# Kernel optimization log

Measured on AMD Instinct MI355X. Metric: run time of the kernel, lower is better.

## Reference

```python
import jax, jax.numpy as jnp
import numpy as np

EPS = 1e-6


def setup_inputs() -> dict:
    key = jax.random.key(0)
    ks = jax.random.split(key, 6)
    B, T, C, H, D, M = 1, 2048, 1024, 16, 64, 64
    return {
        "x": jax.random.normal(ks[0], (B, T, C), dtype=jnp.float32),
        "w_qkv": jax.random.normal(ks[1], (C, 3 * C), dtype=jnp.float32) * (1.0 / np.sqrt(C)),
        "b_qkv": jax.random.normal(ks[2], (3 * C,), dtype=jnp.float32) * 0.02,
        "w_out": jax.random.normal(ks[3], (C, C), dtype=jnp.float32) * (1.0 / np.sqrt(C)),
        "b_out": jax.random.normal(ks[4], (C,), dtype=jnp.float32) * 0.02,
        "proj": jax.random.normal(ks[5], (H, D, M), dtype=jnp.float32),
    }


def _feature_map(x, proj):
    # x: [B,H,T,D], proj: [H,D,M] -> [B,H,T,M]
    M = proj.shape[-1]
    p = jnp.einsum("bhtd,hdm->bhtm", x, proj)
    return jax.nn.relu(p) / jnp.sqrt(jnp.float32(M))


def reference(x, w_qkv, b_qkv, w_out, b_out, proj):
    B, T, C = x.shape
    H, D, M = proj.shape
    qkv = x @ w_qkv + b_qkv                        # [B,T,3C]
    q, k, v = jnp.split(qkv, 3, axis=-1)
    # [B,T,C] -> [B,H,T,D]
    to_heads = lambda t: t.reshape(B, T, H, D).transpose(0, 2, 1, 3)
    q, k, v = to_heads(q), to_heads(k), to_heads(v)

    q_prime = _feature_map(q, proj)                # [B,H,T,M]
    k_prime = _feature_map(k, proj)                # [B,H,T,M]

    # causal linear attention: cumulative sum of outer products k' v^T
    kv_prod = jnp.einsum("bhtm,bhtd->bhtmd", k_prime, v)   # [B,H,T,M,D]
    kv_cumsum = jnp.cumsum(kv_prod, axis=2)
    context = jnp.einsum("bhtm,bhtmd->bhtd", q_prime, kv_cumsum)

    k_cumsum = jnp.cumsum(k_prime, axis=2)                   # [B,H,T,M]
    norm = jnp.einsum("bhtm,bhtm->bht", q_prime, k_cumsum)
    out = context / (norm[..., None] + EPS)                  # [B,H,T,D]

    out = out.transpose(0, 2, 1, 3).reshape(B, T, C)
    return out @ w_out + b_out
```

## Files before the change

### kernel.cpp

```cpp
#include <hip/hip_runtime.h>
#include <hip/hip_bf16.h>

#define TT 2048
#define CC 1024
#define HH 16
#define DD 64
#define FM 64
#define NCH 32
#define CL 64
#define N_QKV 3072
#define EPSV 1e-6f

#define OFF_KS  0u
#define OFF_Z   32768u
#define OFF_U16 65536u
#define U_KVT 0u
#define U_PROJT 2097152u
#define U_VT  6291456u
#define U_QP  8388608u
#define U_KP  10485760u
#define U_ST  12582912u
#define U_XBF 14680064u
#define U_WQT 16777216u
#define U_WOT 19922944u

typedef __attribute__((ext_vector_type(8))) short bf16x8;
typedef __attribute__((ext_vector_type(4))) float f32x4;
typedef __attribute__((ext_vector_type(4))) unsigned short u16x4;

__device__ __forceinline__ unsigned short f2bf(float f) {
  unsigned int u = __float_as_uint(f);
  u = (u + 0x7fffu + ((u >> 16) & 1u)) >> 16;
  return (unsigned short)u;
}
__device__ __forceinline__ float bf2f(unsigned short b) {
  return __uint_as_float(((unsigned)b) << 16);
}

__device__ __forceinline__ void gload16(const void* g, void* l) {
  __builtin_amdgcn_global_load_lds(
      (const __attribute__((address_space(1))) unsigned int*)g,
      (__attribute__((address_space(3))) unsigned int*)l, 16, 0, 0);
}

__device__ __forceinline__ void stage_tile64(const unsigned short* g, unsigned rowstride,
                                             unsigned short* lds, int w, int lane) {
  const int l8 = lane >> 3, l7 = lane & 7;
  const int kcg = (l7 ^ l8) * 8;
#pragma unroll
  for (int jj = 0; jj < 2; ++jj) {
    const int inst = w * 2 + jj;
    const int row = inst * 8 + l8;
    gload16(&g[(unsigned)row * rowstride + kcg], &lds[inst * 512]);
  }
}

__device__ __forceinline__ bf16x8 frag64(const unsigned short* lds, int r, int kchunk) {
  const int slot = kchunk ^ (r & 7);
  return *reinterpret_cast<const bf16x8*>(&lds[r * 64 + slot * 8]);
}

__device__ __forceinline__ void transpose64_dev(const float* __restrict__ src,
                                                unsigned short* __restrict__ dst,
                                                int K, int N, int k0, int n0,
                                                float (*T)[68], int tid) {
#pragma unroll
  for (int it = 0; it < 4; ++it) {
    int f = tid + it * 256;
    int r = f >> 4, c4 = (f & 15) * 4;
    float4 v = *reinterpret_cast<const float4*>(&src[(unsigned)(k0 + r) * N + n0 + c4]);
    T[r][c4 + 0] = v.x; T[r][c4 + 1] = v.y;
    T[r][c4 + 2] = v.z; T[r][c4 + 3] = v.w;
  }
  __syncthreads();
#pragma unroll
  for (int it = 0; it < 4; ++it) {
    int f = tid + it * 256;
    int nl = f >> 4, kq = (f & 15) * 4;
    u16x4 o;
#pragma unroll
    for (int j = 0; j < 4; ++j) o[j] = f2bf(T[kq + j][nl]);
    *reinterpret_cast<u16x4*>(&dst[(unsigned)(n0 + nl) * K + k0 + kq]) = o;
  }
}

__global__ __launch_bounds__(256) void k_prep(const float* __restrict__ x,
                                              const float* __restrict__ wq,
                                              const float* __restrict__ wo,
                                              const float* __restrict__ proj,
                                              unsigned short* __restrict__ xbf,
                                              unsigned short* __restrict__ wqT,
                                              unsigned short* __restrict__ woT,
                                              unsigned short* __restrict__ projT) {
  __shared__ float T[64][68];
  const int tid = threadIdx.x;
  int b = blockIdx.x;
  if (b < 2048) {
    unsigned i = (unsigned)b * 1024u + (unsigned)tid * 4u;
    float4 v = *reinterpret_cast<const float4*>(&x[i]);
    u16x4 o;
    o[0] = f2bf(v.x); o[1] = f2bf(v.y); o[2] = f2bf(v.z); o[3] = f2bf(v.w);
    *reinterpret_cast<u16x4*>(&xbf[i]) = o;
    return;
  }
  b -= 2048;
  if (b < 768) {
    transpose64_dev(wq, wqT, CC, N_QKV, (b / 48) * 64, (b % 48) * 64, T, tid);
    return;
  }
  b -= 768;
  if (b < 256) {
    transpose64_dev(wo, woT, CC, CC, (b / 16) * 64, (b % 16) * 64, T, tid);
    return;
  }
  b -= 256;
  transpose64_dev(proj + (unsigned)b * 4096u, projT + (unsigned)b * 4096u, 64, 64, 0, 0, T, tid);
}

__global__ __launch_bounds__(256) void k_qkv_mfma(const unsigned short* __restrict__ Xbf,
                                                  const unsigned short* __restrict__ WqT,
                                                  const float* __restrict__ bias,
                                                  const unsigned short* __restrict__ projT,
                                                  unsigned short* __restrict__ qp,
                                                  unsigned short* __restrict__ kp,
                                                  unsigned short* __restrict__ vt) {
  __shared__ unsigned short LDSU[12288];
  unsigned short* As = LDSU;
  unsigned short* Bs = LDSU + 4096;
  const int tid = threadIdx.x, lane = tid & 63, w = tid >> 6;
  const int wm = w >> 1, wn = w & 1;
  int lin = blockIdx.y * 24 + blockIdx.x;
  int swz = (lin & 7) * 96 + (lin >> 3);
  const int bx = swz % 24, by = swz / 24;
  const int m0b = by * 64, n0b = bx * 128;
  const int l8 = lane >> 3, l7 = lane & 7;
  const int kcg = (l7 ^ l8) * 8;
  f32x4 acc[2][4] = {};
  for (int k0 = 0; k0 < CC; k0 += 64) {
    if (k0) __syncthreads();
#pragma unroll
    for (int jj = 0; jj < 2; ++jj) {
      const int inst = w * 2 + jj;
      const int row = inst * 8 + l8;
      gload16(&Xbf[(unsigned)(m0b + row) * CC + k0 + kcg], &As[inst * 512]);
    }
#pragma unroll
    for (int jj = 0; jj < 4; ++jj) {
      const int inst = w * 4 + jj;
      const int row = inst * 8 + l8;
      gload16(&WqT[(unsigned)(n0b + row) * CC + k0 + kcg], &Bs[inst * 512]);
    }
    __syncthreads();
#pragma unroll
    for (int kk = 0; kk < 2; ++kk) {
      bf16x8 af[2], bg[4];
#pragma unroll
      for (int i = 0; i < 2; ++i) {
        const int r = wm * 32 + i * 16 + (lane & 15);
        const int slot = (kk * 4 + (lane >> 4)) ^ (r & 7);
        af[i] = *reinterpret_cast<const bf16x8*>(&As[r * 64 + slot * 8]);
      }
#pragma unroll
      for (int j = 0; j < 4; ++j) {
        const int r = wn * 64 + j * 16 + (lane & 15);
        const int slot = (kk * 4 + (lane >> 4)) ^ (r & 7);
        bg[j] = *reinterpret_cast<const bf16x8*>(&Bs[r * 64 + slot * 8]);
      }
#pragma unroll
      for (int i = 0; i < 2; ++i)
#pragma unroll
        for (int j = 0; j < 4; ++j)
          acc[i][j] = __builtin_amdgcn_mfma_f32_16x16x32_bf16(af[i], bg[j],
                                                              acc[i][j], 0, 0, 0);
    }
  }
  const int n0w = n0b + wn * 64;
  const int sel = n0w >> 10;
  const int h = (n0w & 1023) >> 6;
  const int t0w = m0b + wm * 32;
  float bvj[4];
#pragma unroll
  for (int j = 0; j < 4; ++j) bvj[j] = bias[n0w + j * 16 + (lane & 15)];
  __syncthreads();
  unsigned short* myT = LDSU + w * 2048;
#pragma unroll
  for (int i = 0; i < 2; ++i)
#pragma unroll
    for (int j = 0; j < 4; ++j) {
      const int d = j * 16 + (lane & 15);
#pragma unroll
      for (int r = 0; r < 4; ++r) {
        const int t = i * 16 + (lane >> 4) * 4 + r;
        myT[t * 64 + (((d >> 3) ^ (t & 7)) << 3) + (d & 7)] = f2bf(acc[i][j][r] + bvj[j]);
      }
    }
  if (sel == 2) {
#pragma unroll
    for (int q = 0; q < 4; ++q) {
      const int cid = q * 64 + lane;
      const int d = cid >> 2, tc = cid & 3;
      bf16x8 o;
#pragma unroll
      for (int e = 0; e < 8; ++e) {
        const int t = tc * 8 + e;
        o[e] = (short)myT[t * 64 + (((d >> 3) ^ (t & 7)) << 3) + (d & 7)];
      }
      *reinterpret_cast<bf16x8*>(&vt[((unsigned)h * 64 + d) * TT + t0w + tc * 8]) = o;
    }
    return;
  }
  const unsigned short* pjt = projT + (unsigned)h * 4096u;
  bf16x8 aq[2][2], bp[4][2];
#pragma unroll
  for (int jm = 0; jm < 4; ++jm)
#pragma unroll
    for (int kk = 0; kk < 2; ++kk)
      bp[jm][kk] = *reinterpret_cast<const bf16x8*>(
          &pjt[(unsigned)(jm * 16 + (lane & 15)) * 64 + kk * 32 + (lane >> 4) * 8]);
#pragma unroll
  for (int i = 0; i < 2; ++i)
#pragma unroll
    for (int kk = 0; kk < 2; ++kk)
      aq[i][kk] = frag64(myT, i * 16 + (lane & 15), kk * 4 + (lane >> 4));
  f32x4 accp[2][4] = {};
#pragma unroll
  for (int i = 0; i < 2; ++i)
#pragma unroll
    for (int jm = 0; jm < 4; ++jm)
#pragma unroll
      for (int kk = 0; kk < 2; ++kk)
        accp[i][jm] = __builtin_amdgcn_mfma_f32_16x16x32_bf16(aq[i][kk], bp[jm][kk],
                                                              accp[i][jm], 0, 0, 0);
#pragma unroll
  for (int i = 0; i < 2; ++i)
#pragma unroll
    for (int jm = 0; jm < 4; ++jm) {
      const int m = jm * 16 + (lane & 15);
#pragma unroll
      for (int r = 0; r < 4; ++r) {
        const int t = i * 16 + (lane >> 4) * 4 + r;
        float v = accp[i][jm][r];
        v = (v > 0.f ? v : 0.f) * 0.125f;
        myT[t * 64 + (((m >> 3) ^ (t & 7)) << 3) + (m & 7)] = f2bf(v);
      }
    }
  unsigned short* dst0 = (sel ? kp : qp) + ((unsigned)h * TT + (unsigned)t0w) * 64u;
#pragma unroll
  for (int q = 0; q < 4; ++q) {
    const int cid = q * 64 + lane;
    const int t = cid >> 3, mc = cid & 7;
    bf16x8 o = *reinterpret_cast<const bf16x8*>(&myT[t * 64 + ((mc ^ (t & 7)) << 3)]);
    *reinterpret_cast<bf16x8*>(&dst0[(unsigned)cid * 8]) = o;
  }
}

__global__ __launch_bounds__(256) void k_chunkkv(const unsigned short* __restrict__ kp,
                                                 const unsigned short* __restrict__ vt,
                                                 unsigned short* __restrict__ kvt,
                                                 float* __restrict__ ksum) {
  __shared__ unsigned short Xs[4096];
  __shared__ unsigned short VTs[4096];
  const int tid = threadIdx.x, lane = tid & 63, w = tid >> 6;
  const int c = blockIdx.x, h = blockIdx.y;
  stage_tile64(kp + ((unsigned)h * TT + c * 64) * 64, 64, Xs, w, lane);
  stage_tile64(vt + (unsigned)h * 64 * TT + (unsigned)c * 64, TT, VTs, w, lane);
  __syncthreads();
  const int m = w * 16 + (lane & 15);
  bf16x8 afm[2];
  float ks = 0.f;
#pragma unroll
  for (int kk = 0; kk < 2; ++kk)
#pragma unroll
    for (int e = 0; e < 8; ++e) {
      const int t = kk * 32 + (lane >> 4) * 8 + e;
      unsigned short u = Xs[t * 64 + (((m >> 3) ^ (t & 7)) << 3) + (m & 7)];
      afm[kk][e] = (short)u;
      ks += bf2f(u);
    }
  ks += __shfl_xor(ks, 16, 64);
  ks += __shfl_xor(ks, 32, 64);
  if (lane < 16) ksum[((unsigned)h * NCH + c) * 64u + m] = ks;
  f32x4 acckv[4] = {};
#pragma unroll
  for (int j = 0; j < 4; ++j)
#pragma unroll
    for (int kk = 0; kk < 2; ++kk)
      acckv[j] = __builtin_amdgcn_mfma_f32_16x16x32_bf16(
          afm[kk], frag64(VTs, j * 16 + (lane & 15), kk * 4 + (lane >> 4)), acckv[j], 0, 0, 0);
  unsigned short* dkv = kvt + ((unsigned)h * NCH + c) * 4096u;
#pragma unroll
  for (int j = 0; j < 4; ++j) {
    const int d = j * 16 + (lane & 15);
    const int mq = w * 16 + (lane >> 4) * 4;
    u16x4 o;
#pragma unroll
    for (int r = 0; r < 4; ++r) o[r] = f2bf(acckv[j][r]);
    *reinterpret_cast<u16x4*>(&dkv[(unsigned)d * 64 + mq]) = o;
  }
}

__global__ __launch_bounds__(256) void k_prefix(const unsigned short* __restrict__ kvt,
                                                const float* __restrict__ ksum,
                                                unsigned short* __restrict__ st,
                                                float* __restrict__ z) {
  const int h = blockIdx.y;
  const unsigned e = blockIdx.x * 256u + threadIdx.x;
  float run = 0.f;
#pragma unroll
  for (int c = 0; c < NCH; ++c) {
    const unsigned idx = ((unsigned)h * NCH + c) * 4096u + e;
    st[idx] = f2bf(run);
    run += bf2f(kvt[idx]);
  }
  if (blockIdx.x == 0 && threadIdx.x < 64) {
    float zr = 0.f;
#pragma unroll
    for (int c = 0; c < NCH; ++c) {
      const unsigned idx = ((unsigned)h * NCH + c) * 64u + threadIdx.x;
      z[idx] = zr;
      zr += ksum[idx];
    }
  }
}

__global__ __launch_bounds__(256) void k_attn(const unsigned short* __restrict__ qp,
                                              const unsigned short* __restrict__ kp,
                                              const unsigned short* __restrict__ vt,
                                              const unsigned short* __restrict__ st,
                                              const float* __restrict__ z,
                                              unsigned short* __restrict__ attnb) {
  __shared__ unsigned short QPs[4096];
  __shared__ unsigned short KPs[4096];
  __shared__ unsigned short VTs[4096];
  __shared__ unsigned short STs[4096];
  __shared__ float zsm[64];
  __shared__ float nsm[64];
  const int tid = threadIdx.x, lane = tid & 63, w = tid >> 6;
  const int c = blockIdx.x, h = blockIdx.y;
  stage_tile64(qp + ((unsigned)h * TT + c * 64) * 64, 64, QPs, w, lane);
  stage_tile64(kp + ((unsigned)h * TT + c * 64) * 64, 64, KPs, w, lane);
  stage_tile64(vt + (unsigned)h * 64 * TT + (unsigned)c * 64, TT, VTs, w, lane);
  stage_tile64(st + ((unsigned)h * NCH + c) * 4096u, 64, STs, w, lane);
  if (tid < 64) zsm[tid] = z[((unsigned)h * NCH + c) * 64u + tid];
  __syncthreads();
  const int tr = w * 16 + (lane & 15);
  bf16x8 afq[2];
#pragma unroll
  for (int kk = 0; kk < 2; ++kk) afq[kk] = frag64(QPs, tr, kk * 4 + (lane >> 4));
  f32x4 accA[4] = {};
#pragma unroll
  for (int j = 0; j < 4; ++j)
#pragma unroll
    for (int kk = 0; kk < 2; ++kk)
      accA[j] = __builtin_amdgcn_mfma_f32_16x16x32_bf16(
          afq[kk], frag64(KPs, j * 16 + (lane & 15), kk * 4 + (lane >> 4)), accA[j], 0, 0, 0);
  float rs[4] = {0.f, 0.f, 0.f, 0.f};
#pragma unroll
  for (int j = 0; j < 4; ++j) {
    const int s = j * 16 + (lane & 15);
#pragma unroll
    for (int r = 0; r < 4; ++r) {
      const int t = w * 16 + (lane >> 4) * 4 + r;
      float v = (s <= t) ? accA[j][r] : 0.f;
      accA[j][r] = v;
      rs[r] += v;
    }
  }
#pragma unroll
  for (int r = 0; r < 4; ++r)
#pragma unroll
    for (int off = 1; off < 16; off <<= 1) rs[r] += __shfl_xor(rs[r], off, 64);
  __syncthreads();
  if ((lane & 15) == 0) {
#pragma unroll
    for (int r = 0; r < 4; ++r) nsm[w * 16 + (lane >> 4) * 4 + r] = rs[r];
  }
#pragma unroll
  for (int j = 0; j < 4; ++j) {
    const int s = j * 16 + (lane & 15);
#pragma unroll
    for (int r = 0; r < 4; ++r) {
      const int t = w * 16 + (lane >> 4) * 4 + r;
      KPs[t * 64 + (((s >> 3) ^ (t & 7)) * 8) + (s & 7)] = f2bf(accA[j][r]);
    }
  }
  __syncthreads();
  {
    const int t = tid >> 2, part = tid & 3;
    float qz = 0.f;
#pragma unroll
    for (int mm = 0; mm < 16; ++mm) {
      const int m = part * 16 + mm;
      qz += bf2f(QPs[t * 64 + (((m >> 3) ^ (t & 7)) * 8) + (m & 7)]) * zsm[m];
    }
    qz += __shfl_xor(qz, 1, 64);
    qz += __shfl_xor(qz, 2, 64);
    if (part == 0) nsm[t] += qz + EPSV;
  }
  bf16x8 afa[2];
#pragma unroll
  for (int kk = 0; kk < 2; ++kk) afa[kk] = frag64(KPs, tr, kk * 4 + (lane >> 4));
  f32x4 acc[4] = {};
#pragma unroll
  for (int j = 0; j < 4; ++j) {
    const int br = j * 16 + (lane & 15);
#pragma unroll
    for (int kk = 0; kk < 2; ++kk) {
      acc[j] = __builtin_amdgcn_mfma_f32_16x16x32_bf16(
          afa[kk], frag64(VTs, br, kk * 4 + (lane >> 4)), acc[j], 0, 0, 0);
      acc[j] = __builtin_amdgcn_mfma_f32_16x16x32_bf16(
          afq[kk], frag64(STs, br, kk * 4 + (lane >> 4)), acc[j], 0, 0, 0);
    }
  }
  __syncthreads();
#pragma unroll
  for (int j = 0; j < 4; ++j) {
    const int d = j * 16 + (lane & 15);
#pragma unroll
    for (int r = 0; r < 4; ++r) {
      const int t = w * 16 + (lane >> 4) * 4 + r;
      attnb[(unsigned)(c * 64 + t) * CC + h * 64 + d] = f2bf(acc[j][r] / nsm[t]);
    }
  }
}

__global__ __launch_bounds__(256) void k_out_mfma(const unsigned short* __restrict__ Abf,
                                                  const unsigned short* __restrict__ WoT,
                                                  const float* __restrict__ bias,
                                                  float* __restrict__ out) {
  __shared__ unsigned short As[4096];
  __shared__ unsigned short Bs[4096];
  const int tid = threadIdx.x, lane = tid & 63, w = tid >> 6;
  const int wm = w >> 1, wn = w & 1;
  int lin = blockIdx.y * 16 + blockIdx.x;
  int swz = (lin & 7) * 64 + (lin >> 3);
  const int bx = swz & 15, by = swz >> 4;
  const int m0 = by * 64, n0 = bx * 64;
  const int l8 = lane >> 3, l7 = lane & 7;
  const int kcg = (l7 ^ l8) * 8;
  f32x4 acc[2][2] = {};
  for (int k0 = 0; k0 < CC; k0 += 64) {
    if (k0) __syncthreads();
#pragma unroll
    for (int jj = 0; jj < 2; ++jj) {
      const int inst = w * 2 + jj;
      const int row = inst * 8 + l8;
      gload16(&Abf[(unsigned)(m0 + row) * CC + k0 + kcg], &As[inst * 512]);
      gload16(&WoT[(unsigned)(n0 + row) * CC + k0 + kcg], &Bs[inst * 512]);
    }
    __syncthreads();
#pragma unroll
    for (int kk = 0; kk < 2; ++kk) {
      bf16x8 af[2], bg[2];
#pragma unroll
      for (int i = 0; i < 2; ++i) {
        const int r = wm * 32 + i * 16 + (lane & 15);
        const int slot = (kk * 4 + (lane >> 4)) ^ (r & 7);
        af[i] = *reinterpret_cast<const bf16x8*>(&As[r * 64 + slot * 8]);
      }
#pragma unroll
      for (int j = 0; j < 2; ++j) {
        const int r = wn * 32 + j * 16 + (lane & 15);
        const int slot = (kk * 4 + (lane >> 4)) ^ (r & 7);
        bg[j] = *reinterpret_cast<const bf16x8*>(&Bs[r * 64 + slot * 8]);
      }
#pragma unroll
      for (int i = 0; i < 2; ++i)
#pragma unroll
        for (int j = 0; j < 2; ++j)
          acc[i][j] = __builtin_amdgcn_mfma_f32_16x16x32_bf16(af[i], bg[j],
                                                              acc[i][j], 0, 0, 0);
    }
  }
#pragma unroll
  for (int i = 0; i < 2; ++i) {
#pragma unroll
    for (int j = 0; j < 2; ++j) {
      const int n = n0 + wn * 32 + j * 16 + (lane & 15);
      const float bv = bias[n];
#pragma unroll
      for (int r = 0; r < 4; ++r) {
        const int m = m0 + wm * 32 + i * 16 + (lane >> 4) * 4 + r;
        out[(unsigned)m * CC + n] = acc[i][j][r] + bv;
      }
    }
  }
}

extern "C" void kernel_launch(void* const* d_in, const int* in_sizes, int n_in,
                              void* d_out, int out_size, void* d_ws, size_t ws_size,
                              hipStream_t stream) {
  const float* x = (const float*)d_in[0];
  const float* w_qkv = (const float*)d_in[1];
  const float* b_qkv = (const float*)d_in[2];
  const float* w_out = (const float*)d_in[3];
  const float* b_out = (const float*)d_in[4];
  const float* proj = (const float*)d_in[5];
  float* ws = (float*)d_ws;
  float* out = (float*)d_out;
  float* ksum = ws + OFF_KS;
  float* zf = ws + OFF_Z;
  unsigned short* ub = (unsigned short*)(ws + OFF_U16);
  unsigned short* kvt = ub + U_KVT;
  unsigned short* projT = ub + U_PROJT;
  unsigned short* vt = ub + U_VT;
  unsigned short* qp = ub + U_QP;
  unsigned short* kp = ub + U_KP;
  unsigned short* st = ub + U_ST;
  unsigned short* xbf = ub + U_XBF;
  unsigned short* wqT = ub + U_WQT;
  unsigned short* woT = ub + U_WOT;
  unsigned short* attnb = xbf;
  dim3 blk(256, 1, 1);
  k_prep<<<dim3(3088), blk, 0, stream>>>(x, w_qkv, w_out, proj, xbf, wqT, woT, projT);
  k_qkv_mfma<<<dim3(N_QKV / 128, TT / 64), blk, 0, stream>>>(xbf, wqT, b_qkv, projT,
                                                             qp, kp, vt);
  k_chunkkv<<<dim3(NCH, HH), blk, 0, stream>>>(kp, vt, kvt, ksum);
  k_prefix<<<dim3(16, HH), blk, 0, stream>>>(kvt, ksum, st, zf);
  k_attn<<<dim3(NCH, HH), blk, 0, stream>>>(qp, kp, vt, st, zf, attnb);
  k_out_mfma<<<dim3(CC / 64, TT / 64), blk, 0, stream>>>(attnb, woT, b_out, out);
}
```

Before: 68.92 us.

## Fuse all stages into one cooperative persistent kernel with grid syncs

Wraps every stage (prep, QKV GEMM, chunk KV, prefix, attention, output GEMM) as device functions and runs them inside one cooperative kernel of 768 blocks separated by grid.sync, removing five kernel launch gaps. It falls back to the six separate launches when cooperative launch or occupancy of at least 3 blocks per CU is not available. The attention epilogue now stages its output through LDS and writes coalesced 16-byte rows. Costs include grid-wide barrier latency, idle blocks in the smaller stages, and a larger shared LDS allocation that may limit occupancy. It also calls host attribute and occupancy queries on every launch.

```diff
diff --git a/kernel.cpp b/kernel.cpp
--- a/kernel.cpp
+++ b/kernel.cpp
@@ -1,5 +1,8 @@
 #include <hip/hip_runtime.h>
 #include <hip/hip_bf16.h>
+#include <hip/hip_cooperative_groups.h>
+
+namespace cg = cooperative_groups;
 
 #define TT 2048
 #define CC 1024
@@ -60,6 +63,7 @@
   return *reinterpret_cast<const bf16x8*>(&lds[r * 64 + slot * 8]);
 }
 
+
 __device__ __forceinline__ void transpose64_dev(const float* __restrict__ src,
                                                 unsigned short* __restrict__ dst,
                                                 int K, int N, int k0, int n0,
@@ -84,52 +88,47 @@
   }
 }
 
-__global__ __launch_bounds__(256) void k_prep(const float* __restrict__ x,
-                                              const float* __restrict__ wq,
-                                              const float* __restrict__ wo,
-                                              const float* __restrict__ proj,
-                                              unsigned short* __restrict__ xbf,
-                                              unsigned short* __restrict__ wqT,
-                                              unsigned short* __restrict__ woT,
-                                              unsigned short* __restrict__ projT) {
-  __shared__ float T[64][68];
+__device__ __forceinline__ void prep_item(int b, const float* __restrict__ x,
+                                          const float* __restrict__ wq,
+                                          const float* __restrict__ wo,
+                                          const float* __restrict__ proj,
+                                          unsigned short* __restrict__ xbf,
+                                          unsigned short* __restrict__ wqT,
+                                          unsigned short* __restrict__ woT,
+                                          unsigned short* __restrict__ projT,
+                                          float (*T)[68]) {
   const int tid = threadIdx.x;
-  int b = blockIdx.x;
   if (b < 2048) {
     unsigned i = (unsigned)b * 1024u + (unsigned)tid * 4u;
     float4 v = *reinterpret_cast<const float4*>(&x[i]);
     u16x4 o;
     o[0] = f2bf(v.x); o[1] = f2bf(v.y); o[2] = f2bf(v.z); o[3] = f2bf(v.w);
     *reinterpret_cast<u16x4*>(&xbf[i]) = o;
-    return;
-  }
-  b -= 2048;
-  if (b < 768) {
-    transpose64_dev(wq, wqT, CC, N_QKV, (b / 48) * 64, (b % 48) * 64, T, tid);
-    return;
-  }
-  b -= 768;
-  if (b < 256) {
-    transpose64_dev(wo, woT, CC, CC, (b / 16) * 64, (b % 16) * 64, T, tid);
-    return;
-  }
-  b -= 256;
-  transpose64_dev(proj + (unsigned)b * 4096u, projT + (unsigned)b * 4096u, 64, 64, 0, 0, T, tid);
-}
-
-__global__ __launch_bounds__(256) void k_qkv_mfma(const unsigned short* __restrict__ Xbf,
-                                                  const unsigned short* __restrict__ WqT,
-                                                  const float* __restrict__ bias,
-                                                  const unsigned short* __restrict__ projT,
-                                                  unsigned short* __restrict__ qp,
-                                                  unsigned short* __restrict__ kp,
-                                                  unsigned short* __restrict__ vt) {
-  __shared__ unsigned short LDSU[12288];
+  } else if (b < 2816) {
+    int bb = b - 2048;
+    transpose64_dev(wq, wqT, CC, N_QKV, (bb / 48) * 64, (bb % 48) * 64, T, tid);
+  } else if (b < 3072) {
+    int bb = b - 2816;
+    transpose64_dev(wo, woT, CC, CC, (bb / 16) * 64, (bb % 16) * 64, T, tid);
+  } else {
+    int bb = b - 3072;
+    transpose64_dev(proj + (unsigned)bb * 4096u, projT + (unsigned)bb * 4096u,
+                    64, 64, 0, 0, T, tid);
+  }
+}
+
+__device__ __forceinline__ void qkv_body(int lin, const unsigned short* __restrict__ Xbf,
+                                         const unsigned short* __restrict__ WqT,
+                                         const float* __restrict__ bias,
+                                         const unsigned short* __restrict__ projT,
+                                         unsigned short* __restrict__ qp,
+                                         unsigned short* __restrict__ kp,
+                                         unsigned short* __restrict__ vt,
+                                         unsigned short* LDSU) {
   unsigned short* As = LDSU;
   unsigned short* Bs = LDSU + 4096;
   const int tid = threadIdx.x, lane = tid & 63, w = tid >> 6;
   const int wm = w >> 1, wn = w & 1;
-  int lin = blockIdx.y * 24 + blockIdx.x;
   int swz = (lin & 7) * 96 + (lin >> 3);
   const int bx = swz % 24, by = swz / 24;
   const int m0b = by * 64, n0b = bx * 128;
@@ -207,61 +206,62 @@
       }
       *reinterpret_cast<bf16x8*>(&vt[((unsigned)h * 64 + d) * TT + t0w + tc * 8]) = o;
     }
-    return;
-  }
-  const unsigned short* pjt = projT + (unsigned)h * 4096u;
-  bf16x8 aq[2][2], bp[4][2];
-#pragma unroll
-  for (int jm = 0; jm < 4; ++jm)
-#pragma unroll
-    for (int kk = 0; kk < 2; ++kk)
-      bp[jm][kk] = *reinterpret_cast<const bf16x8*>(
-          &pjt[(unsigned)(jm * 16 + (lane & 15)) * 64 + kk * 32 + (lane >> 4) * 8]);
-#pragma unroll
-  for (int i = 0; i < 2; ++i)
-#pragma unroll
-    for (int kk = 0; kk < 2; ++kk)
-      aq[i][kk] = frag64(myT, i * 16 + (lane & 15), kk * 4 + (lane >> 4));
-  f32x4 accp[2][4] = {};
-#pragma unroll
-  for (int i = 0; i < 2; ++i)
+  } else {
+    const unsigned short* pjt = projT + (unsigned)h * 4096u;
+    bf16x8 aq[2][2], bp[4][2];
 #pragma unroll
     for (int jm = 0; jm < 4; ++jm)
 #pragma unroll
       for (int kk = 0; kk < 2; ++kk)
-        accp[i][jm] = __builtin_amdgcn_mfma_f32_16x16x32_bf16(aq[i][kk], bp[jm][kk],
-                                                              accp[i][jm], 0, 0, 0);
-#pragma unroll
-  for (int i = 0; i < 2; ++i)
-#pragma unroll
-    for (int jm = 0; jm < 4; ++jm) {
-      const int m = jm * 16 + (lane & 15);
-#pragma unroll
-      for (int r = 0; r < 4; ++r) {
-        const int t = i * 16 + (lane >> 4) * 4 + r;
-        float v = accp[i][jm][r];
-        v = (v > 0.f ? v : 0.f) * 0.125f;
-        myT[t * 64 + (((m >> 3) ^ (t & 7)) << 3) + (m & 7)] = f2bf(v);
-      }
-    }
-  unsigned short* dst0 = (sel ? kp : qp) + ((unsigned)h * TT + (unsigned)t0w) * 64u;
-#pragma unroll
-  for (int q = 0; q < 4; ++q) {
-    const int cid = q * 64 + lane;
-    const int t = cid >> 3, mc = cid & 7;
-    bf16x8 o = *reinterpret_cast<const bf16x8*>(&myT[t * 64 + ((mc ^ (t & 7)) << 3)]);
-    *reinterpret_cast<bf16x8*>(&dst0[(unsigned)cid * 8]) = o;
-  }
-}
-
-__global__ __launch_bounds__(256) void k_chunkkv(const unsigned short* __restrict__ kp,
-                                                 const unsigned short* __restrict__ vt,
-                                                 unsigned short* __restrict__ kvt,
-                                                 float* __restrict__ ksum) {
-  __shared__ unsigned short Xs[4096];
-  __shared__ unsigned short VTs[4096];
+        bp[jm][kk] = *reinterpret_cast<const bf16x8*>(
+            &pjt[(unsigned)(jm * 16 + (lane & 15)) * 64 + kk * 32 + (lane >> 4) * 8]);
+#pragma unroll
+    for (int i = 0; i < 2; ++i)
+#pragma unroll
+      for (int kk = 0; kk < 2; ++kk)
+        aq[i][kk] = frag64(myT, i * 16 + (lane & 15), kk * 4 + (lane >> 4));
+    f32x4 accp[2][4] = {};
+#pragma unroll
+    for (int i = 0; i < 2; ++i)
+#pragma unroll
+      for (int jm = 0; jm < 4; ++jm)
+#pragma unroll
+        for (int kk = 0; kk < 2; ++kk)
+          accp[i][jm] = __builtin_amdgcn_mfma_f32_16x16x32_bf16(aq[i][kk], bp[jm][kk],
+                                                                accp[i][jm], 0, 0, 0);
+#pragma unroll
+    for (int i = 0; i < 2; ++i)
+#pragma unroll
+      for (int jm = 0; jm < 4; ++jm) {
+        const int m = jm * 16 + (lane & 15);
+#pragma unroll
+        for (int r = 0; r < 4; ++r) {
+          const int t = i * 16 + (lane >> 4) * 4 + r;
+          float v = accp[i][jm][r];
+          v = (v > 0.f ? v : 0.f) * 0.125f;
+          myT[t * 64 + (((m >> 3) ^ (t & 7)) << 3) + (m & 7)] = f2bf(v);
+        }
+      }
+    unsigned short* dst0 = (sel ? kp : qp) + ((unsigned)h * TT + (unsigned)t0w) * 64u;
+#pragma unroll
+    for (int q = 0; q < 4; ++q) {
+      const int cid = q * 64 + lane;
+      const int t = cid >> 3, mc = cid & 7;
+      bf16x8 o = *reinterpret_cast<const bf16x8*>(&myT[t * 64 + ((mc ^ (t & 7)) << 3)]);
+      *reinterpret_cast<bf16x8*>(&dst0[(unsigned)cid * 8]) = o;
+    }
+  }
+}
+
+__device__ __forceinline__ void chunkkv_body(int c, int h,
+                                             const unsigned short* __restrict__ kp,
+                                             const unsigned short* __restrict__ vt,
+                                             unsigned short* __restrict__ kvt,
+                                             float* __restrict__ ksum,
+                                             unsigned short* LDSU) {
+  unsigned short* Xs = LDSU;
+  unsigned short* VTs = LDSU + 4096;
   const int tid = threadIdx.x, lane = tid & 63, w = tid >> 6;
-  const int c = blockIdx.x, h = blockIdx.y;
   stage_tile64(kp + ((unsigned)h * TT + c * 64) * 64, 64, Xs, w, lane);
   stage_tile64(vt + (unsigned)h * 64 * TT + (unsigned)c * 64, TT, VTs, w, lane);
   __syncthreads();
@@ -299,12 +299,12 @@
   }
 }
 
-__global__ __launch_bounds__(256) void k_prefix(const unsigned short* __restrict__ kvt,
-                                                const float* __restrict__ ksum,
-                                                unsigned short* __restrict__ st,
-                                                float* __restrict__ z) {
-  const int h = blockIdx.y;
-  const unsigned e = blockIdx.x * 256u + threadIdx.x;
+__device__ __forceinline__ void prefix_body(int bxp, int h,
+                                            const unsigned short* __restrict__ kvt,
+                                            const float* __restrict__ ksum,
+                                            unsigned short* __restrict__ st,
+                                            float* __restrict__ z) {
+  const unsigned e = (unsigned)bxp * 256u + threadIdx.x;
   float run = 0.f;
 #pragma unroll
   for (int c = 0; c < NCH; ++c) {
@@ -312,7 +312,7 @@
     st[idx] = f2bf(run);
     run += bf2f(kvt[idx]);
   }
-  if (blockIdx.x == 0 && threadIdx.x < 64) {
+  if (bxp == 0 && threadIdx.x < 64) {
     float zr = 0.f;
 #pragma unroll
     for (int c = 0; c < NCH; ++c) {
@@ -323,20 +323,21 @@
   }
 }
 
-__global__ __launch_bounds__(256) void k_attn(const unsigned short* __restrict__ qp,
-                                              const unsigned short* __restrict__ kp,
-                                              const unsigned short* __restrict__ vt,
-                                              const unsigned short* __restrict__ st,
-                                              const float* __restrict__ z,
-                                              unsigned short* __restrict__ attnb) {
-  __shared__ unsigned short QPs[4096];
-  __shared__ unsigned short KPs[4096];
-  __shared__ unsigned short VTs[4096];
-  __shared__ unsigned short STs[4096];
-  __shared__ float zsm[64];
-  __shared__ float nsm[64];
+__device__ __forceinline__ void attn_body(int c, int h,
+                                          const unsigned short* __restrict__ qp,
+                                          const unsigned short* __restrict__ kp,
+                                          const unsigned short* __restrict__ vt,
+                                          const unsigned short* __restrict__ st,
+                                          const float* __restrict__ z,
+                                          unsigned short* __restrict__ attnb,
+                                          unsigned short* LDSU) {
+  unsigned short* QPs = LDSU;
+  unsigned short* KPs = LDSU + 4096;
+  unsigned short* VTs = LDSU + 8192;
+  unsigned short* STs = LDSU + 12288;
+  float* zsm = (float*)(LDSU + 16384);
+  float* nsm = zsm + 64;
   const int tid = threadIdx.x, lane = tid & 63, w = tid >> 6;
-  const int c = blockIdx.x, h = blockIdx.y;
   stage_tile64(qp + ((unsigned)h * TT + c * 64) * 64, 64, QPs, w, lane);
   stage_tile64(kp + ((unsigned)h * TT + c * 64) * 64, 64, KPs, w, lane);
   stage_tile64(vt + (unsigned)h * 64 * TT + (unsigned)c * 64, TT, VTs, w, lane);
@@ -419,20 +420,29 @@
 #pragma unroll
     for (int r = 0; r < 4; ++r) {
       const int t = w * 16 + (lane >> 4) * 4 + r;
-      attnb[(unsigned)(c * 64 + t) * CC + h * 64 + d] = f2bf(acc[j][r] / nsm[t]);
-    }
-  }
-}
-
-__global__ __launch_bounds__(256) void k_out_mfma(const unsigned short* __restrict__ Abf,
-                                                  const unsigned short* __restrict__ WoT,
-                                                  const float* __restrict__ bias,
-                                                  float* __restrict__ out) {
-  __shared__ unsigned short As[4096];
-  __shared__ unsigned short Bs[4096];
+      QPs[t * 64 + (((d >> 3) ^ (t & 7)) << 3) + (d & 7)] = f2bf(acc[j][r] / nsm[t]);
+    }
+  }
+  __syncthreads();
+  unsigned short* dstA = attnb + (unsigned)(c * 64) * CC + (unsigned)h * 64;
+#pragma unroll
+  for (int q = 0; q < 2; ++q) {
+    const int cid = q * 256 + tid;
+    const int t = cid >> 3, dc = cid & 7;
+    bf16x8 o = *reinterpret_cast<const bf16x8*>(&QPs[t * 64 + ((dc ^ (t & 7)) << 3)]);
+    *reinterpret_cast<bf16x8*>(&dstA[(unsigned)t * CC + dc * 8]) = o;
+  }
+}
+
+__device__ __forceinline__ void out_body(int lin, const unsigned short* __restrict__ Abf,
+                                         const unsigned short* __restrict__ WoT,
+                                         const float* __restrict__ bias,
+                                         float* __restrict__ out,
+                                         unsigned short* LDSU) {
+  unsigned short* As = LDSU;
+  unsigned short* Bs = LDSU + 4096;
   const int tid = threadIdx.x, lane = tid & 63, w = tid >> 6;
   const int wm = w >> 1, wn = w & 1;
-  int lin = blockIdx.y * 16 + blockIdx.x;
   int swz = (lin & 7) * 64 + (lin >> 3);
   const int bx = swz & 15, by = swz >> 4;
   const int m0 = by * 64, n0 = bx * 64;
@@ -485,6 +495,83 @@
       }
     }
   }
+}
+
+
+__global__ __launch_bounds__(256) void k_prep(const float* x, const float* wq,
+                                              const float* wo, const float* proj,
+                                              unsigned short* xbf, unsigned short* wqT,
+                                              unsigned short* woT, unsigned short* projT) {
+  __shared__ float T[64][68];
+  prep_item(blockIdx.x, x, wq, wo, proj, xbf, wqT, woT, projT, T);
+}
+
+__global__ __launch_bounds__(256) void k_qkv_mfma(const unsigned short* Xbf,
+                                                  const unsigned short* WqT,
+                                                  const float* bias,
+                                                  const unsigned short* projT,
+                                                  unsigned short* qp, unsigned short* kp,
+                                                  unsigned short* vt) {
+  __shared__ unsigned short LDSU[12288];
+  qkv_body(blockIdx.y * 24 + blockIdx.x, Xbf, WqT, bias, projT, qp, kp, vt, LDSU);
+}
+
+__global__ __launch_bounds__(256) void k_chunkkv(const unsigned short* kp,
+                                                 const unsigned short* vt,
+                                                 unsigned short* kvt, float* ksum) {
+  __shared__ unsigned short LDSU[8192];
+  chunkkv_body(blockIdx.x, blockIdx.y, kp, vt, kvt, ksum, LDSU);
+}
+
+__global__ __launch_bounds__(256) void k_prefix(const unsigned short* kvt,
+                                                const float* ksum,
+                                                unsigned short* st, float* z) {
+  prefix_body(blockIdx.x, blockIdx.y, kvt, ksum, st, z);
+}
+
+__global__ __launch_bounds__(256) void k_attn(const unsigned short* qp,
+                                              const unsigned short* kp,
+                                              const unsigned short* vt,
+                                              const unsigned short* st,
+                                              const float* z, unsigned short* attnb) {
+  __shared__ unsigned short LDSU[16640];
+  attn_body(blockIdx.x, blockIdx.y, qp, kp, vt, st, z, attnb, LDSU);
+}
+
+__global__ __launch_bounds__(256) void k_out_mfma(const unsigned short* Abf,
+                                                  const unsigned short* WoT,
+                                                  const float* bias, float* out) {
+  __shared__ unsigned short LDSU[8192];
+  out_body(blockIdx.y * 16 + blockIdx.x, Abf, WoT, bias, out, LDSU);
+}
+
+
+__global__ __launch_bounds__(256, 3) void k_mega(const float* x, const float* wq,
+                                                 const float* wo, const float* proj,
+                                                 const float* bq, const float* bo,
+                                                 unsigned short* xbf, unsigned short* wqT,
+                                                 unsigned short* woT, unsigned short* projT,
+                                                 unsigned short* qp, unsigned short* kp,
+                                                 unsigned short* vt, unsigned short* kvt,
+                                                 float* ksum, unsigned short* st, float* zf,
+                                                 unsigned short* attnb, float* out) {
+  __shared__ __align__(16) unsigned short LDSU[16640];
+  cg::grid_group grid = cg::this_grid();
+  const int blk = blockIdx.x;
+  for (int b = blk; b < 3088; b += 768) {
+    prep_item(b, x, wq, wo, proj, xbf, wqT, woT, projT, (float(*)[68])LDSU);
+    __syncthreads();
+  }
+  grid.sync();
+  qkv_body(blk, xbf, wqT, bq, projT, qp, kp, vt, LDSU);
+  grid.sync();
+  if (blk < 512) chunkkv_body(blk & 31, blk >> 5, kp, vt, kvt, ksum, LDSU);
+  grid.sync();
+  if (blk < 256) prefix_body(blk & 15, blk >> 4, kvt, ksum, st, zf);
+  grid.sync();
+  if (blk < 512) attn_body(blk & 31, blk >> 5, qp, kp, vt, st, zf, attnb, LDSU);
+  grid.sync();
+  if (blk < 512) out_body(blk, attnb, woT, bo, out, LDSU);
 }
 
 extern "C" void kernel_launch(void* const* d_in, const int* in_sizes, int n_in,
@@ -511,12 +598,29 @@
   unsigned short* wqT = ub + U_WQT;
   unsigned short* woT = ub + U_WOT;
   unsigned short* attnb = xbf;
-  dim3 blk(256, 1, 1);
-  k_prep<<<dim3(3088), blk, 0, stream>>>(x, w_qkv, w_out, proj, xbf, wqT, woT, projT);
-  k_qkv_mfma<<<dim3(N_QKV / 128, TT / 64), blk, 0, stream>>>(xbf, wqT, b_qkv, projT,
-                                                             qp, kp, vt);
-  k_chunkkv<<<dim3(NCH, HH), blk, 0, stream>>>(kp, vt, kvt, ksum);
-  k_prefix<<<dim3(16, HH), blk, 0, stream>>>(kvt, ksum, st, zf);
-  k_attn<<<dim3(NCH, HH), blk, 0, stream>>>(qp, kp, vt, st, zf, attnb);
-  k_out_mfma<<<dim3(CC / 64, TT / 64), blk, 0, stream>>>(attnb, woT, b_out, out);
-}
+
+  int dev = 0;
+  hipGetDevice(&dev);
+  int coop = 0;
+  hipDeviceGetAttribute(&coop, hipDeviceAttributeCooperativeLaunch, dev);
+  int nb = 0;
+  hipOccupancyMaxActiveBlocksPerMultiprocessor(&nb, k_mega, 256, 0);
+
+  if (coop && nb >= 3) {
+    void* args[] = {(void*)&x, (void*)&w_qkv, (void*)&w_out, (void*)&proj,
+                    (void*)&b_qkv, (void*)&b_out,
+                    (void*)&xbf, (void*)&wqT, (void*)&woT, (void*)&projT,
+                    (void*)&qp, (void*)&kp, (void*)&vt, (void*)&kvt,
+                    (void*)&ksum, (void*)&st, (void*)&zf, (void*)&attnb, (void*)&out};
+    hipLaunchCooperativeKernel((void*)k_mega, dim3(768), dim3(256), args, 0, stream);
+  } else {
+    dim3 blk(256, 1, 1);
+    k_prep<<<dim3(3088), blk, 0, stream>>>(x, w_qkv, w_out, proj, xbf, wqT, woT, projT);
+    k_qkv_mfma<<<dim3(N_QKV / 128, TT / 64), blk, 0, stream>>>(xbf, wqT, b_qkv, projT,
+                                                               qp, kp, vt);
+    k_chunkkv<<<dim3(NCH, HH), blk, 0, stream>>>(kp, vt, kvt, ksum);
+    k_prefix<<<dim3(16, HH), blk, 0, stream>>>(kvt, ksum, st, zf);
+    k_attn<<<dim3(NCH, HH), blk, 0, stream>>>(qp, kp, vt, st, zf, attnb);
+    k_out_mfma<<<dim3(CC / 64, TT / 64), blk, 0, stream>>>(attnb, woT, b_out, out);
+  }
+}
```

After: 69.00 us. Within noise of the previous version (+0.1%).
